# Kernel tuning notes

Hardware: AMD Instinct MI355X
Metric: run time of the kernel (lower is better)

The kernel has to match this reference:

```python
import jax, jax.numpy as jnp
import numpy as np

N_HEADS = 16
WINDOW = 128
EPS = 1e-6
NEG_INF = -1e30  # effectively -inf after softmax in fp32


def setup_inputs() -> dict:
    key = jax.random.key(0)
    ks = jax.random.split(key, 5)
    B, T, D = 2, 2048, 1024
    scale = 1.0 / np.sqrt(D)
    return {
        "x": jax.random.normal(ks[0], (B, T, D), dtype=jnp.float32),
        "Wq": jax.random.normal(ks[1], (D, D), dtype=jnp.float32) * scale,
        "Wk": jax.random.normal(ks[2], (D, D), dtype=jnp.float32) * scale,
        "Wv": jax.random.normal(ks[3], (D, D), dtype=jnp.float32) * scale,
        "Wo": jax.random.normal(ks[4], (D, D), dtype=jnp.float32) * scale,
    }


def _l2norm(t):
    # torch F.normalize: t / max(||t||, eps)
    n = jnp.sqrt(jnp.sum(t * t, axis=-1, keepdims=True))
    return t / jnp.maximum(n, EPS)


def reference(x, Wq, Wk, Wv, Wo):
    B, T, D = x.shape
    H, hd = N_HEADS, D // N_HEADS
    # projections (torch Linear: x @ W.T), split heads -> [B, H, T, hd]
    def proj(W):
        return jnp.einsum('btd,ed->bte', x, W).reshape(B, T, H, hd).transpose(0, 2, 1, 3)
    q = _l2norm(proj(Wq))
    k = _l2norm(proj(Wk))
    v = proj(Wv)
    # scores [B, H, T, T] (no 1/sqrt(d) scale in the source)
    attn = jnp.einsum('bhqd,bhkd->bhqk', q, k)
    pos = jnp.arange(T)
    rel = pos[None, :] - pos[:, None]            # rel[i, j] = j - i
    mask = (rel < 0) | (rel >= WINDOW)           # allowed: 0 <= j-i < window
    base = jnp.linspace(0.0, 1.0, H, dtype=x.dtype)
    slopes = jnp.power(jnp.asarray(2.0, x.dtype), -(8.0 * base))  # [H]
    alibi = -jnp.abs(rel).astype(x.dtype)[None, :, :] * slopes[:, None, None]  # [H,T,T]
    bias = jnp.where(mask[None, :, :], jnp.asarray(NEG_INF, x.dtype), alibi)
    attn = jax.nn.softmax(attn + bias[None], axis=-1)
    out = jnp.einsum('bhqk,bhkd->bhqd', attn, v)
    out = out.transpose(0, 2, 1, 3).reshape(B, T, D)
    return jnp.einsum('btd,ed->bte', out, Wo)
```

## Files before the change

### kernel.cpp

```cpp
#include <hip/hip_runtime.h>
#include <hip/hip_bf16.h>

#define T_SEQ   2048
#define BATCH   2
#define DMODEL  1024
#define NHEADS  16
#define HDIM    64
#define WINDOW  128

typedef __attribute__((ext_vector_type(8))) short bf16x8;
typedef __attribute__((ext_vector_type(4))) float f32x4;

__device__ inline void gld_lds16(const __hip_bfloat16* g, __hip_bfloat16* l) {
    __builtin_amdgcn_global_load_lds(
        (const __attribute__((address_space(1))) unsigned int*)g,
        (__attribute__((address_space(3))) unsigned int*)l, 16, 0, 0);
}

__device__ inline bf16x8 ds_readb128(const __hip_bfloat16* p) {
    bf16x8 r;
    asm volatile("ds_read_b128 %0, %1"
                 : "=v"(r)
                 : "v"((const __attribute__((address_space(3))) __hip_bfloat16*)p));
    return r;
}

__global__ __launch_bounds__(256) void cvt_kernel(
    const float* __restrict__ x,  const float* __restrict__ Wq,
    const float* __restrict__ Wk, const float* __restrict__ Wv,
    const float* __restrict__ Wo,
    __hip_bfloat16* __restrict__ xb, __hip_bfloat16* __restrict__ Wb)
{
    const int lid = blockIdx.x;
    const float* src;
    __hip_bfloat16* dst;
    int blk;
    if (lid < 2048) { src = x; dst = xb; blk = lid; }
    else {
        int slot = (lid - 2048) >> 9;
        blk = (lid - 2048) & 511;
        src = (slot == 0) ? Wq : (slot == 1) ? Wk : (slot == 2) ? Wv : Wo;
        dst = Wb + (size_t)slot * 1024 * 1024;
    }
    int i = (blk * 256 + threadIdx.x) * 8;
    float4 a = *(const float4*)(src + i);
    float4 b = *(const float4*)(src + i + 4);
    __hip_bfloat16 pk[8] = {
        __float2bfloat16(a.x), __float2bfloat16(a.y),
        __float2bfloat16(a.z), __float2bfloat16(a.w),
        __float2bfloat16(b.x), __float2bfloat16(b.y),
        __float2bfloat16(b.z), __float2bfloat16(b.w)};
    *(uint4*)(dst + i) = *(uint4*)pk;
}

__device__ inline void stageA(const __hip_bfloat16* __restrict__ A,
                              __hip_bfloat16* dst, int m0, int k0, int half,
                              int w, int lane)
{
#pragma unroll
    for (int i = 0; i < 2; ++i) {
        int g0   = w * 16 + i * 8;
        int row0 = (g0 & 63) + ((g0 >> 6) << 7) + (half << 6);
        int r    = row0 + (lane >> 3);
        int gcx  = ((lane & 7) - r) & 7;
        gld_lds16(A + (size_t)(m0 + r) * DMODEL + k0 + gcx * 8, dst + row0 * 64);
    }
}

__device__ inline void stageB(const __hip_bfloat16* __restrict__ W,
                              __hip_bfloat16* dst, int n0, int k0, int half,
                              int w, int lane)
{
#pragma unroll
    for (int i = 0; i < 2; ++i) {
        int g0   = w * 16 + i * 8;
        int row0 = (g0 & 31) + ((g0 >> 5) << 6) + (half << 5);
        int r    = row0 + (lane >> 3);
        int gcx  = ((lane & 7) - r) & 7;
        gld_lds16(W + (size_t)(n0 + r) * DMODEL + k0 + gcx * 8, dst + row0 * 64);
    }
}

__device__ inline bf16x8 rdfrag(const __hip_bfloat16* buf, int r, int kc) {
    return ds_readb128(&buf[r * 64 + (((kc + r) & 7) << 3)]);
}

__global__ __launch_bounds__(512, 2) void gemm_qkv(
    const __hip_bfloat16* __restrict__ A,
    const __hip_bfloat16* __restrict__ Wp,
    __hip_bfloat16* __restrict__ C0,
    __hip_bfloat16* __restrict__ C1,
    __hip_bfloat16* __restrict__ C2)
{
    const int lid   = blockIdx.x;
    const int wgid  = (lid & 7) * 24 + (lid >> 3);
    const int bn    = wgid % 12;
    const int bm    = wgid / 12;
    const int m0    = bm * 256;
    const int n0    = bn * 256;
    const int z     = n0 >> 10;
    const int cbase = n0 & 1023;

    __shared__ __hip_bfloat16 As[2][256 * 64];
    __shared__ __hip_bfloat16 Bs[2][256 * 64];

    const int t    = threadIdx.x;
    const int lane = t & 63;
    const int w    = t >> 6;
    const int wr   = w >> 2;
    const int wc   = w & 3;
    const int lrow = lane & 15;
    const int quad = lane >> 4;
    const int arow = wr * 128;
    const int brow = wc * 64;

    f32x4 acc[8][4];
#pragma unroll
    for (int i = 0; i < 8; ++i)
#pragma unroll
        for (int j = 0; j < 4; ++j)
            acc[i][j] = (f32x4){0.f, 0.f, 0.f, 0.f};

    stageA(A,  As[0], m0, 0, 0, w, lane);
    stageB(Wp, Bs[0], n0, 0, 0, w, lane);
    stageB(Wp, Bs[0], n0, 0, 1, w, lane);
    stageA(A,  As[0], m0, 0, 1, w, lane);
    asm volatile("s_waitcnt vmcnt(4)" ::: "memory");
    __builtin_amdgcn_s_barrier();

    bf16x8 af[4][2];
    bf16x8 bfr[2][2];

    for (int tt = 0; tt < 16; ++tt) {
        const int p  = tt & 1;
        const int pn = p ^ 1;
        const __hip_bfloat16* Ar = As[p];
        const __hip_bfloat16* Br = Bs[p];
        const int k1   = (tt + 1) << 6;
        const bool pf  = (tt < 15);

#pragma unroll
        for (int mi = 0; mi < 4; ++mi) {
            int r = arow + mi * 16 + lrow;
            af[mi][0] = rdfrag(Ar, r, quad);
            af[mi][1] = rdfrag(Ar, r, 4 + quad);
        }
#pragma unroll
        for (int ni = 0; ni < 2; ++ni) {
            int r = brow + ni * 16 + lrow;
            bfr[ni][0] = rdfrag(Br, r, quad);
            bfr[ni][1] = rdfrag(Br, r, 4 + quad);
        }
        if (pf) stageA(A, As[pn], m0, k1, 0, w, lane);
        __builtin_amdgcn_s_barrier();
        asm volatile("s_waitcnt lgkmcnt(0)" ::: "memory");
        __builtin_amdgcn_sched_barrier(0);
        __builtin_amdgcn_s_setprio(1);
#pragma unroll
        for (int mi = 0; mi < 4; ++mi)
#pragma unroll
            for (int ni = 0; ni < 2; ++ni) {
                acc[mi][ni] = __builtin_amdgcn_mfma_f32_16x16x32_bf16(
                    af[mi][0], bfr[ni][0], acc[mi][ni], 0, 0, 0);
                acc[mi][ni] = __builtin_amdgcn_mfma_f32_16x16x32_bf16(
                    af[mi][1], bfr[ni][1], acc[mi][ni], 0, 0, 0);
            }
        __builtin_amdgcn_s_setprio(0);
        asm volatile("s_waitcnt vmcnt(4)" ::: "memory");
        __builtin_amdgcn_s_barrier();

#pragma unroll
        for (int ni = 0; ni < 2; ++ni) {
            int r = brow + (ni + 2) * 16 + lrow;
            bfr[ni][0] = rdfrag(Br, r, quad);
            bfr[ni][1] = rdfrag(Br, r, 4 + quad);
        }
        if (pf) stageB(Wp, Bs[pn], n0, k1, 0, w, lane);
        __builtin_amdgcn_s_barrier();
        asm volatile("s_waitcnt lgkmcnt(0)" ::: "memory");
        __builtin_amdgcn_sched_barrier(0);
        __builtin_amdgcn_s_setprio(1);
#pragma unroll
        for (int mi = 0; mi < 4; ++mi)
#pragma unroll
            for (int ni = 0; ni < 2; ++ni) {
                acc[mi][ni + 2] = __builtin_amdgcn_mfma_f32_16x16x32_bf16(
                    af[mi][0], bfr[ni][0], acc[mi][ni + 2], 0, 0, 0);
                acc[mi][ni + 2] = __builtin_amdgcn_mfma_f32_16x16x32_bf16(
                    af[mi][1], bfr[ni][1], acc[mi][ni + 2], 0, 0, 0);
            }
        __builtin_amdgcn_s_setprio(0);
        asm volatile("s_waitcnt vmcnt(4)" ::: "memory");
        __builtin_amdgcn_s_barrier();

#pragma unroll
        for (int mi = 0; mi < 4; ++mi) {
            int r = arow + (mi + 4) * 16 + lrow;
            af[mi][0] = rdfrag(Ar, r, quad);
            af[mi][1] = rdfrag(Ar, r, 4 + quad);
        }
#pragma unroll
        for (int ni = 0; ni < 2; ++ni) {
            int r = brow + ni * 16 + lrow;
            bfr[ni][0] = rdfrag(Br, r, quad);
            bfr[ni][1] = rdfrag(Br, r, 4 + quad);
        }
        if (pf) stageB(Wp, Bs[pn], n0, k1, 1, w, lane);
        __builtin_amdgcn_s_barrier();
        asm volatile("s_waitcnt lgkmcnt(0)" ::: "memory");
        __builtin_amdgcn_sched_barrier(0);
        __builtin_amdgcn_s_setprio(1);
#pragma unroll
        for (int mi = 0; mi < 4; ++mi)
#pragma unroll
            for (int ni = 0; ni < 2; ++ni) {
                acc[mi + 4][ni] = __builtin_amdgcn_mfma_f32_16x16x32_bf16(
                    af[mi][0], bfr[ni][0], acc[mi + 4][ni], 0, 0, 0);
                acc[mi + 4][ni] = __builtin_amdgcn_mfma_f32_16x16x32_bf16(
                    af[mi][1], bfr[ni][1], acc[mi + 4][ni], 0, 0, 0);
            }
        __builtin_amdgcn_s_setprio(0);
        __builtin_amdgcn_s_barrier();

#pragma unroll
        for (int ni = 0; ni < 2; ++ni) {
            int r = brow + (ni + 2) * 16 + lrow;
            bfr[ni][0] = rdfrag(Br, r, quad);
            bfr[ni][1] = rdfrag(Br, r, 4 + quad);
        }
        if (pf) stageA(A, As[pn], m0, k1, 1, w, lane);
        __builtin_amdgcn_s_barrier();
        asm volatile("s_waitcnt lgkmcnt(0)" ::: "memory");
        __builtin_amdgcn_sched_barrier(0);
        __builtin_amdgcn_s_setprio(1);
#pragma unroll
        for (int mi = 0; mi < 4; ++mi)
#pragma unroll
            for (int ni = 0; ni < 2; ++ni) {
                acc[mi + 4][ni + 2] = __builtin_amdgcn_mfma_f32_16x16x32_bf16(
                    af[mi][0], bfr[ni][0], acc[mi + 4][ni + 2], 0, 0, 0);
                acc[mi + 4][ni + 2] = __builtin_amdgcn_mfma_f32_16x16x32_bf16(
                    af[mi][1], bfr[ni][1], acc[mi + 4][ni + 2], 0, 0, 0);
            }
        __builtin_amdgcn_s_setprio(0);
        asm volatile("s_waitcnt vmcnt(4)" ::: "memory");
        __builtin_amdgcn_s_barrier();
    }

    if (z != 2) {
#pragma unroll
        for (int mi = 0; mi < 8; ++mi) {
#pragma unroll
            for (int rr = 0; rr < 4; ++rr) {
                float ss = 0.f;
#pragma unroll
                for (int ni = 0; ni < 4; ++ni)
                    ss += acc[mi][ni][rr] * acc[mi][ni][rr];
                ss += __shfl_xor(ss, 1);
                ss += __shfl_xor(ss, 2);
                ss += __shfl_xor(ss, 4);
                ss += __shfl_xor(ss, 8);
                float inv = 1.0f / fmaxf(sqrtf(ss), 1e-6f);
#pragma unroll
                for (int ni = 0; ni < 4; ++ni)
                    acc[mi][ni][rr] *= inv;
            }
        }
    }

    __hip_bfloat16* C = (z == 0) ? C0 : (z == 1) ? C1 : C2;
#pragma unroll
    for (int mi = 0; mi < 8; ++mi) {
#pragma unroll
        for (int rr = 0; rr < 4; ++rr) {
            int row = m0 + arow + mi * 16 + quad * 4 + rr;
            __hip_bfloat16* Crow = C + (size_t)row * DMODEL + cbase + brow + lrow;
#pragma unroll
            for (int ni = 0; ni < 4; ++ni)
                Crow[ni * 16] = __float2bfloat16(acc[mi][ni][rr]);
        }
    }
}

__global__ __launch_bounds__(256) void gemm_o(
    const __hip_bfloat16* __restrict__ A,
    const __hip_bfloat16* __restrict__ W,
    float* __restrict__ C,
    int M, int N, int K)
{
    const int lid   = blockIdx.x + 8 * blockIdx.y;
    const int xcd   = lid & 7;
    const int s     = lid >> 3;
    const int m_loc = s & 15;
    const int n_loc = s >> 4;

    const int m0 = ((xcd & 3) * 16 + m_loc) * 64;
    const int n0 = ((xcd >> 2) * 4 + n_loc) * 128;

    __shared__ __hip_bfloat16 As[64 * 64];
    __shared__ __hip_bfloat16 Bs[128 * 64];

    const int t    = threadIdx.x;
    const int lane = t & 63;
    const int wv   = t >> 6;

    const int drow = lane >> 3;
    const int sl   = lane & 7;

    const int wm   = (wv >> 1) * 32;
    const int wn   = (wv & 1) * 64;
    const int lrow = lane & 15;
    const int quad = lane >> 4;

    f32x4 acc[2][4];
#pragma unroll
    for (int i = 0; i < 2; i++)
#pragma unroll
        for (int j = 0; j < 4; j++)
            acc[i][j] = (f32x4){0.f, 0.f, 0.f, 0.f};

    for (int k0 = 0; k0 < K; k0 += 64) {
#pragma unroll
        for (int inst = 0; inst < 2; inst++) {
            int r0 = wv * 16 + inst * 8;
            int r  = r0 + drow;
            int gcx = (sl - r) & 7;
            gld_lds16(A + (size_t)(m0 + r) * K + k0 + gcx * 8, &As[r0 * 64]);
        }
#pragma unroll
        for (int inst = 0; inst < 4; inst++) {
            int r0 = wv * 32 + inst * 8;
            int r  = r0 + drow;
            int gcx = (sl - r) & 7;
            gld_lds16(W + (size_t)(n0 + r) * K + k0 + gcx * 8, &Bs[r0 * 64]);
        }
        __syncthreads();

#pragma unroll
        for (int kk = 0; kk < 2; kk++) {
            bf16x8 af[2], bfv[4];
#pragma unroll
            for (int mi = 0; mi < 2; mi++) {
                int r = wm + mi * 16 + lrow;
                af[mi] = *(const bf16x8*)&As[r * 64 + ((kk * 4 + quad + r) & 7) * 8];
            }
#pragma unroll
            for (int ni = 0; ni < 4; ni++) {
                int r = wn + ni * 16 + lrow;
                bfv[ni] = *(const bf16x8*)&Bs[r * 64 + ((kk * 4 + quad + r) & 7) * 8];
            }
#pragma unroll
            for (int mi = 0; mi < 2; mi++)
#pragma unroll
                for (int ni = 0; ni < 4; ni++)
                    acc[mi][ni] = __builtin_amdgcn_mfma_f32_16x16x32_bf16(
                        af[mi], bfv[ni], acc[mi][ni], 0, 0, 0);
        }
        __syncthreads();
    }

#pragma unroll
    for (int mi = 0; mi < 2; mi++) {
#pragma unroll
        for (int rr = 0; rr < 4; rr++) {
            int row = m0 + wm + mi * 16 + quad * 4 + rr;
            float* Crow = C + (size_t)row * N + n0 + wn + lrow;
#pragma unroll
            for (int ni = 0; ni < 4; ni++)
                Crow[ni * 16] = acc[mi][ni][rr];
        }
    }
}

__global__ __launch_bounds__(512) void attn_kernel(
    const __hip_bfloat16* __restrict__ Q,
    const __hip_bfloat16* __restrict__ K,
    const __hip_bfloat16* __restrict__ V,
    __hip_bfloat16* __restrict__ O)
{
    const int qb = blockIdx.x * 128;
    const int h  = blockIdx.y;
    const int b  = blockIdx.z;

    __shared__ __hip_bfloat16 KsP[8 * 16 * 168];
    __shared__ __hip_bfloat16 Vt[64 * 264];

    const size_t base = ((size_t)b * T_SEQ) * DMODEL + h * HDIM;
    const int t    = threadIdx.x;
    const int lane = t & 63;
    const int w    = t >> 6;

    {
        const int drow = lane >> 3, sl = lane & 7;
#pragma unroll
        for (int inst = 0; inst < 4; inst++) {
            int r0 = w * 32 + inst * 8;
            int r  = r0 + drow;
            int gcx = (sl - r) & 7;
            int j  = min(qb + r, T_SEQ - 1);
            gld_lds16(K + base + (size_t)j * DMODEL + gcx * 8, &KsP[r0 * 64]);
        }
    }
    if (t < 256) {
        int c  = t & 7;
        int b0 = t >> 3;
        int sg = (b0 & ~7) | ((b0 + c) & 7);
        unsigned short m[8][8];
#pragma unroll
        for (int i = 0; i < 8; i++) {
            int j = min(qb + b0 * 8 + i, T_SEQ - 1);
            uint4 u = *(const uint4*)(V + base + (size_t)j * DMODEL + c * 8);
            unsigned short tmp[8];
            *(uint4*)tmp = u;
#pragma unroll
            for (int e = 0; e < 8; e++) m[e][i] = tmp[e];
        }
#pragma unroll
        for (int e = 0; e < 8; e++)
            *(uint4*)&Vt[(c * 8 + e) * 264 + sg * 8] = *(uint4*)m[e];
    }
    if (t < 64) {
        uint4 zz = {0, 0, 0, 0};
        *(uint4*)&Vt[t * 264 + 256] = zz;
    }
    __syncthreads();

    const int col  = lane & 15;
    const int quad = lane >> 4;
    const float slope = exp2f(-8.0f * (float)h / 15.0f);

    const __hip_bfloat16* qp = Q + base + (size_t)(qb + w * 16 + col) * DMODEL + quad * 8;
    bf16x8 qf0 = *(const bf16x8*)(qp);
    bf16x8 qf1 = *(const bf16x8*)(qp + 32);

    f32x4 sc[9];
#pragma unroll
    for (int kt = 0; kt < 9; kt++) {
        sc[kt] = (f32x4){0.f, 0.f, 0.f, 0.f};
        int r = w * 16 + kt * 16 + col;
        bf16x8 kb0 = *(const bf16x8*)&KsP[r * 64 + ((quad     + r) & 7) * 8];
        bf16x8 kb1 = *(const bf16x8*)&KsP[r * 64 + ((quad + 4 + r) & 7) * 8];
        sc[kt] = __builtin_amdgcn_mfma_f32_16x16x32_bf16(qf0, kb0, sc[kt], 0, 0, 0);
        sc[kt] = __builtin_amdgcn_mfma_f32_16x16x32_bf16(qf1, kb1, sc[kt], 0, 0, 0);
    }

    float mx[4] = {-3e38f, -3e38f, -3e38f, -3e38f};
#pragma unroll
    for (int kt = 0; kt < 9; kt++) {
#pragma unroll
        for (int r = 0; r < 4; r++) {
            int ql  = quad * 4 + r;
            int rel = kt * 16 + col - ql;
            int ka  = qb + w * 16 + kt * 16 + col;
            bool valid = (rel >= 0) && (rel < WINDOW) && (ka < T_SEQ);
            float v = valid ? (sc[kt][r] - (float)rel * slope) : -1e30f;
            sc[kt][r] = v;
            mx[r] = fmaxf(mx[r], v);
        }
    }
#pragma unroll
    for (int r = 0; r < 4; r++) {
        mx[r] = fmaxf(mx[r], __shfl_xor(mx[r], 1));
        mx[r] = fmaxf(mx[r], __shfl_xor(mx[r], 2));
        mx[r] = fmaxf(mx[r], __shfl_xor(mx[r], 4));
        mx[r] = fmaxf(mx[r], __shfl_xor(mx[r], 8));
    }
    float sm[4] = {0.f, 0.f, 0.f, 0.f};
#pragma unroll
    for (int kt = 0; kt < 9; kt++) {
#pragma unroll
        for (int r = 0; r < 4; r++) {
            float e = __expf(sc[kt][r] - mx[r]);
            sc[kt][r] = e;
            sm[r] += e;
        }
    }
#pragma unroll
    for (int r = 0; r < 4; r++) {
        sm[r] += __shfl_xor(sm[r], 1);
        sm[r] += __shfl_xor(sm[r], 2);
        sm[r] += __shfl_xor(sm[r], 4);
        sm[r] += __shfl_xor(sm[r], 8);
        sm[r] = 1.0f / sm[r];
    }

    __syncthreads();
    __hip_bfloat16* Ps = KsP + w * (16 * 168);
#pragma unroll
    for (int kt = 0; kt < 9; kt++)
#pragma unroll
        for (int r = 0; r < 4; r++)
            Ps[(quad * 4 + r) * 168 + kt * 16 + col] = __float2bfloat16(sc[kt][r] * sm[r]);
#pragma unroll
    for (int i = 0; i < 4; i++)
        Ps[(lane & 15) * 168 + 144 + quad * 4 + i] = __float2bfloat16(0.f);
    __syncthreads();

    f32x4 o[4];
#pragma unroll
    for (int nd = 0; nd < 4; nd++) o[nd] = (f32x4){0.f, 0.f, 0.f, 0.f};
#pragma unroll
    for (int kc = 0; kc < 5; kc++) {
        bf16x8 pf = *(const bf16x8*)&Ps[col * 168 + kc * 32 + quad * 8];
        int bblk = w * 2 + kc * 4 + quad;
#pragma unroll
        for (int nd = 0; nd < 4; nd++) {
            int d  = nd * 16 + col;
            int sg = (bblk < 32) ? ((bblk & ~7) | ((bblk + (d >> 3)) & 7)) : 32;
            bf16x8 vf = *(const bf16x8*)&Vt[d * 264 + sg * 8];
            o[nd] = __builtin_amdgcn_mfma_f32_16x16x32_bf16(pf, vf, o[nd], 0, 0, 0);
        }
    }

#pragma unroll
    for (int r = 0; r < 4; r++) {
        __hip_bfloat16* op = O + base + (size_t)(qb + w * 16 + quad * 4 + r) * DMODEL + col;
#pragma unroll
        for (int nd = 0; nd < 4; nd++)
            op[nd * 16] = __float2bfloat16(o[nd][r]);
    }
}

extern "C" void kernel_launch(void* const* d_in, const int* in_sizes, int n_in,
                              void* d_out, int out_size, void* d_ws, size_t ws_size,
                              hipStream_t stream)
{
    const float* x  = (const float*)d_in[0];
    const float* Wq = (const float*)d_in[1];
    const float* Wk = (const float*)d_in[2];
    const float* Wv = (const float*)d_in[3];
    const float* Wo = (const float*)d_in[4];
    float* out = (float*)d_out;

    const size_t MT = (size_t)BATCH * T_SEQ;
    __hip_bfloat16* Qw = (__hip_bfloat16*)d_ws;
    __hip_bfloat16* Kw = Qw + MT * DMODEL;
    __hip_bfloat16* Vw = Kw + MT * DMODEL;
    __hip_bfloat16* XA = Vw + MT * DMODEL;
    __hip_bfloat16* Wb = XA + MT * DMODEL;

    cvt_kernel<<<4096, 256, 0, stream>>>(x, Wq, Wk, Wv, Wo, XA, Wb);

    gemm_qkv<<<dim3(192), 512, 0, stream>>>(XA, Wb, Qw, Kw, Vw);

    dim3 g2(T_SEQ / 128, NHEADS, BATCH);
    attn_kernel<<<g2, 512, 0, stream>>>(Qw, Kw, Vw, XA);

    dim3 g3(DMODEL / 128, MT / 64, 1);
    gemm_o<<<g3, 256, 0, stream>>>(
        XA, Wb + 3 * 1024 * 1024, out, (int)MT, DMODEL, DMODEL);
}
```

Measured before the change: 151.0 us.

## Restructure QKV GEMM main loop into k-half phases with register fragment prefetch

Rewrites the projection GEMM inner loop so each k-tile is processed as four MFMA phases split by k-half and M-half. All global-to-LDS staging for the next tile is issued at the start of the iteration. LDS fragment reads for the next phase are issued before the current MFMA batch, with partial lgkmcnt waits, and the next tile's first fragments are prefetched at the end of the loop. This cuts the per-iteration barriers from about eight to two and overlaps LDS reads with MFMA work, at the cost of more live fragment registers and a full vmcnt(0) wait mid-iteration.

After: 155.5 us. 3.0% more time.

```diff
diff --git a/kernel.cpp b/kernel.cpp
--- a/kernel.cpp
+++ b/kernel.cpp
@@ -125,125 +125,104 @@
     stageB(Wp, Bs[0], n0, 0, 0, w, lane);
     stageB(Wp, Bs[0], n0, 0, 1, w, lane);
     stageA(A,  As[0], m0, 0, 1, w, lane);
-    asm volatile("s_waitcnt vmcnt(4)" ::: "memory");
+    asm volatile("s_waitcnt vmcnt(0)" ::: "memory");
     __builtin_amdgcn_s_barrier();
 
-    bf16x8 af[4][2];
-    bf16x8 bfr[2][2];
+    bf16x8 aLa[4], aHa[4], aLb[4], aHb[4], bA[4], bB[4];
+
+#pragma unroll
+    for (int mi = 0; mi < 4; ++mi)
+        aLa[mi] = rdfrag(As[0], arow + mi * 16 + lrow, quad);
+#pragma unroll
+    for (int ni = 0; ni < 4; ++ni)
+        bA[ni] = rdfrag(Bs[0], brow + ni * 16 + lrow, quad);
+    asm volatile("s_waitcnt lgkmcnt(0)" ::: "memory");
+    __builtin_amdgcn_sched_barrier(0);
 
     for (int tt = 0; tt < 16; ++tt) {
         const int p  = tt & 1;
         const int pn = p ^ 1;
         const __hip_bfloat16* Ar = As[p];
         const __hip_bfloat16* Br = Bs[p];
-        const int k1   = (tt + 1) << 6;
-        const bool pf  = (tt < 15);
-
-#pragma unroll
-        for (int mi = 0; mi < 4; ++mi) {
-            int r = arow + mi * 16 + lrow;
-            af[mi][0] = rdfrag(Ar, r, quad);
-            af[mi][1] = rdfrag(Ar, r, 4 + quad);
-        }
-#pragma unroll
-        for (int ni = 0; ni < 2; ++ni) {
-            int r = brow + ni * 16 + lrow;
-            bfr[ni][0] = rdfrag(Br, r, quad);
-            bfr[ni][1] = rdfrag(Br, r, 4 + quad);
-        }
-        if (pf) stageA(A, As[pn], m0, k1, 0, w, lane);
-        __builtin_amdgcn_s_barrier();
-        asm volatile("s_waitcnt lgkmcnt(0)" ::: "memory");
+        const bool pf = (tt < 15);
+        const __hip_bfloat16* Arn = pf ? As[pn] : As[p];
+        const __hip_bfloat16* Brn = pf ? Bs[pn] : Bs[p];
+        const int k1 = pf ? ((tt + 1) << 6) : 0;
+
+        if (pf) {
+            stageA(A,  As[pn], m0, k1, 0, w, lane);
+            stageB(Wp, Bs[pn], n0, k1, 0, w, lane);
+            stageB(Wp, Bs[pn], n0, k1, 1, w, lane);
+            stageA(A,  As[pn], m0, k1, 1, w, lane);
+        }
+#pragma unroll
+        for (int mi = 0; mi < 4; ++mi)
+            aHa[mi] = rdfrag(Ar, arow + (mi + 4) * 16 + lrow, quad);
+
+        __builtin_amdgcn_s_setprio(1);
+#pragma unroll
+        for (int mi = 0; mi < 4; ++mi)
+#pragma unroll
+            for (int ni = 0; ni < 4; ++ni)
+                acc[mi][ni] = __builtin_amdgcn_mfma_f32_16x16x32_bf16(
+                    aLa[mi], bA[ni], acc[mi][ni], 0, 0, 0);
+        __builtin_amdgcn_s_setprio(0);
+
+#pragma unroll
+        for (int mi = 0; mi < 4; ++mi)
+            aLb[mi] = rdfrag(Ar, arow + mi * 16 + lrow, 4 + quad);
+#pragma unroll
+        for (int ni = 0; ni < 4; ++ni)
+            bB[ni] = rdfrag(Br, brow + ni * 16 + lrow, 4 + quad);
+
+        asm volatile("s_waitcnt lgkmcnt(8)" ::: "memory");
         __builtin_amdgcn_sched_barrier(0);
         __builtin_amdgcn_s_setprio(1);
 #pragma unroll
         for (int mi = 0; mi < 4; ++mi)
 #pragma unroll
-            for (int ni = 0; ni < 2; ++ni) {
-                acc[mi][ni] = __builtin_amdgcn_mfma_f32_16x16x32_bf16(
-                    af[mi][0], bfr[ni][0], acc[mi][ni], 0, 0, 0);
-                acc[mi][ni] = __builtin_amdgcn_mfma_f32_16x16x32_bf16(
-                    af[mi][1], bfr[ni][1], acc[mi][ni], 0, 0, 0);
-            }
+            for (int ni = 0; ni < 4; ++ni)
+                acc[mi + 4][ni] = __builtin_amdgcn_mfma_f32_16x16x32_bf16(
+                    aHa[mi], bA[ni], acc[mi + 4][ni], 0, 0, 0);
         __builtin_amdgcn_s_setprio(0);
-        asm volatile("s_waitcnt vmcnt(4)" ::: "memory");
+
+        asm volatile("s_waitcnt vmcnt(0)" ::: "memory");
         __builtin_amdgcn_s_barrier();
 
 #pragma unroll
-        for (int ni = 0; ni < 2; ++ni) {
-            int r = brow + (ni + 2) * 16 + lrow;
-            bfr[ni][0] = rdfrag(Br, r, quad);
-            bfr[ni][1] = rdfrag(Br, r, 4 + quad);
-        }
-        if (pf) stageB(Wp, Bs[pn], n0, k1, 0, w, lane);
-        __builtin_amdgcn_s_barrier();
-        asm volatile("s_waitcnt lgkmcnt(0)" ::: "memory");
+        for (int mi = 0; mi < 4; ++mi)
+            aHb[mi] = rdfrag(Ar, arow + (mi + 4) * 16 + lrow, 4 + quad);
+
+        asm volatile("s_waitcnt lgkmcnt(4)" ::: "memory");
         __builtin_amdgcn_sched_barrier(0);
         __builtin_amdgcn_s_setprio(1);
 #pragma unroll
         for (int mi = 0; mi < 4; ++mi)
 #pragma unroll
-            for (int ni = 0; ni < 2; ++ni) {
-                acc[mi][ni + 2] = __builtin_amdgcn_mfma_f32_16x16x32_bf16(
-                    af[mi][0], bfr[ni][0], acc[mi][ni + 2], 0, 0, 0);
-                acc[mi][ni + 2] = __builtin_amdgcn_mfma_f32_16x16x32_bf16(
-                    af[mi][1], bfr[ni][1], acc[mi][ni + 2], 0, 0, 0);
-            }
+            for (int ni = 0; ni < 4; ++ni)
+                acc[mi][ni] = __builtin_amdgcn_mfma_f32_16x16x32_bf16(
+                    aLb[mi], bB[ni], acc[mi][ni], 0, 0, 0);
         __builtin_amdgcn_s_setprio(0);
-        asm volatile("s_waitcnt vmcnt(4)" ::: "memory");
-        __builtin_amdgcn_s_barrier();
-
-#pragma unroll
-        for (int mi = 0; mi < 4; ++mi) {
-            int r = arow + (mi + 4) * 16 + lrow;
-            af[mi][0] = rdfrag(Ar, r, quad);
-            af[mi][1] = rdfrag(Ar, r, 4 + quad);
-        }
-#pragma unroll
-        for (int ni = 0; ni < 2; ++ni) {
-            int r = brow + ni * 16 + lrow;
-            bfr[ni][0] = rdfrag(Br, r, quad);
-            bfr[ni][1] = rdfrag(Br, r, 4 + quad);
-        }
-        if (pf) stageB(Wp, Bs[pn], n0, k1, 1, w, lane);
-        __builtin_amdgcn_s_barrier();
-        asm volatile("s_waitcnt lgkmcnt(0)" ::: "memory");
+
+#pragma unroll
+        for (int mi = 0; mi < 4; ++mi)
+            aLa[mi] = rdfrag(Arn, arow + mi * 16 + lrow, quad);
+#pragma unroll
+        for (int ni = 0; ni < 4; ++ni)
+            bA[ni] = rdfrag(Brn, brow + ni * 16 + lrow, quad);
+
+        asm volatile("s_waitcnt lgkmcnt(8)" ::: "memory");
         __builtin_amdgcn_sched_barrier(0);
         __builtin_amdgcn_s_setprio(1);
 #pragma unroll
         for (int mi = 0; mi < 4; ++mi)
 #pragma unroll
-            for (int ni = 0; ni < 2; ++ni) {
+            for (int ni = 0; ni < 4; ++ni)
                 acc[mi + 4][ni] = __builtin_amdgcn_mfma_f32_16x16x32_bf16(
-                    af[mi][0], bfr[ni][0], acc[mi + 4][ni], 0, 0, 0);
-                acc[mi + 4][ni] = __builtin_amdgcn_mfma_f32_16x16x32_bf16(
-                    af[mi][1], bfr[ni][1], acc[mi + 4][ni], 0, 0, 0);
-            }
+                    aHb[mi], bB[ni], acc[mi + 4][ni], 0, 0, 0);
         __builtin_amdgcn_s_setprio(0);
-        __builtin_amdgcn_s_barrier();
-
-#pragma unroll
-        for (int ni = 0; ni < 2; ++ni) {
-            int r = brow + (ni + 2) * 16 + lrow;
-            bfr[ni][0] = rdfrag(Br, r, quad);
-            bfr[ni][1] = rdfrag(Br, r, 4 + quad);
-        }
-        if (pf) stageA(A, As[pn], m0, k1, 1, w, lane);
-        __builtin_amdgcn_s_barrier();
+
         asm volatile("s_waitcnt lgkmcnt(0)" ::: "memory");
-        __builtin_amdgcn_sched_barrier(0);
-        __builtin_amdgcn_s_setprio(1);
-#pragma unroll
-        for (int mi = 0; mi < 4; ++mi)
-#pragma unroll
-            for (int ni = 0; ni < 2; ++ni) {
-                acc[mi + 4][ni + 2] = __builtin_amdgcn_mfma_f32_16x16x32_bf16(
-                    af[mi][0], bfr[ni][0], acc[mi + 4][ni + 2], 0, 0, 0);
-                acc[mi + 4][ni + 2] = __builtin_amdgcn_mfma_f32_16x16x32_bf16(
-                    af[mi][1], bfr[ni][1], acc[mi + 4][ni + 2], 0, 0, 0);
-            }
-        __builtin_amdgcn_s_setprio(0);
-        asm volatile("s_waitcnt vmcnt(4)" ::: "memory");
         __builtin_amdgcn_s_barrier();
     }
 
```
